# Kernel tuning notes

Measured on AMD Instinct MI355X. Metric: run time of the kernel, lower is better.

Reference implementation:

```python
import jax, jax.numpy as jnp
import numpy as np

B, LATENT, H, OUT, T, L = 4096, 128, 256, 88, 64, 5  # batch, latent, hidden, output(88 keys), seq_len, num_layers


def setup_inputs() -> dict:
    key = jax.random.key(0)
    ks = jax.random.split(key, 8)
    sc = 1.0 / np.sqrt(H)
    n = lambda k, shp, s: (jax.random.normal(k, shp, jnp.float32) * s)
    return {
        "x": jax.random.normal(ks[0], (B, LATENT), jnp.float32),
        "linear_w": n(ks[1], (H, LATENT), 1.0 / np.sqrt(LATENT)),
        "linear_b": jnp.zeros((H,), jnp.float32),
        # PyTorch LSTM layout: [4H, in] with gate order i, f, g, o. Layer-0 input size == H.
        "w_ih": n(ks[2], (L, 4 * H, H), sc),
        "w_hh": n(ks[3], (L, 4 * H, H), sc),
        "b_ih": n(ks[4], (L, 4 * H), sc),
        "b_hh": n(ks[5], (L, 4 * H), sc),
        "out_w": n(ks[6], (OUT, H), sc),
        "out_b": jnp.zeros((OUT,), jnp.float32),
    }


def _lstm_cell(gates, c):
    # gates: [B, 4H] pre-activation, PyTorch order i, f, g, o
    i, f, g, o = jnp.split(gates, 4, axis=-1)
    c_new = jax.nn.sigmoid(f) * c + jax.nn.sigmoid(i) * jnp.tanh(g)
    h_new = jax.nn.sigmoid(o) * jnp.tanh(c_new)
    return h_new, c_new


def _lstm(xp, w_ih, w_hh, b_ih, b_hh):
    # xp: [B, H] latent projection, repeated over T timesteps (constant input).
    bsz = xp.shape[0]
    gx0 = xp @ w_ih[0].T + b_ih[0]  # layer-0 input gates, constant across time [B, 4H]
    h0 = jnp.zeros((L, bsz, H), xp.dtype)
    c0 = jnp.zeros((L, bsz, H), xp.dtype)

    def step(carry, _):
        h, c = carry  # [L, B, H]
        hs, cs = [], []
        layer_in_gates = gx0
        for l in range(L):  # fixed small loop over structurally distinct layers
            if l > 0:
                layer_in_gates = hs[-1] @ w_ih[l].T + b_ih[l]
            gates = layer_in_gates + h[l] @ w_hh[l].T + b_hh[l]
            hl, cl = _lstm_cell(gates, c[l])
            hs.append(hl)
            cs.append(cl)
        return (jnp.stack(hs), jnp.stack(cs)), hs[-1]

    _, ys = jax.lax.scan(step, (h0, c0), None, length=T)  # ys: [T, B, H]
    return ys.transpose(1, 0, 2)  # [B, T, H]


def reference(x, linear_w, linear_b, w_ih, w_hh, b_ih, b_hh, out_w, out_b):
    xp = x @ linear_w.T + linear_b  # [B, H]; unsqueeze+repeat folded into constant gx0
    y = _lstm(xp, w_ih, w_hh, b_ih, b_hh)  # [B, T, H]
    return jax.nn.sigmoid(y @ out_w.T + out_b)  # [B, T, OUT]
```

## Files before the change

### kernel.cpp

```cpp
#include <hip/hip_runtime.h>
#include <hip/hip_bf16.h>
#include <cstdint>

#define B_ 4096
#define H_ 256
#define G_ 1024
#define T_ 64
#define L_ 5

typedef __hip_bfloat16 bf16;
typedef __bf16 bf16x8 __attribute__((ext_vector_type(8)));
typedef float f32x4 __attribute__((ext_vector_type(4)));

#define OFF_WCOMB   0ull
#define OFF_WIH0R   5242880ull
#define OFF_LWT     5767168ull
#define OFF_XB      5832704ull
#define OFF_OBW     6881280ull
#define OFF_BIAS    6930432ull
#define OFF_W1      6950912ull
#define OFF_B0X     7213056ull
#define OFF_H0      25825280ull
#define OFF_H1      34213888ull
#define OFF_C1      42602496ull
#define OFF_YS      63574016ull
#define OFF_C0      199888896ull
#define TOTAL_WS    220860416ull
#define ZERO_BYTES  31457280ull
#define SLOT_H      2097152ull
#define SLOT_C      4194304ull

__device__ __forceinline__ bf16* h_ptr(char* ws, int l, int p) {
  return (bf16*)(ws + (p ? OFF_H1 : OFF_H0) + (size_t)l * SLOT_H);
}
__device__ __forceinline__ float* c_ptr(char* ws, int l, int p) {
  return (float*)(ws + (p ? OFF_C1 : OFF_C0) + (size_t)l * SLOT_C);
}
__device__ __forceinline__ bf16* ys_ptr(char* ws, int s) {
  return (bf16*)(ws + OFF_YS + (size_t)s * SLOT_H);
}

__device__ __forceinline__ float frcp(float x) { return __builtin_amdgcn_rcpf(x); }
__device__ __forceinline__ float fsig(float x) { return frcp(1.0f + __expf(-x)); }
__device__ __forceinline__ float ftanh(float x) { return 1.0f - 2.0f * frcp(1.0f + __expf(2.0f * x)); }

__device__ __forceinline__ void gload16(const void* g, void* l) {
  __builtin_amdgcn_global_load_lds((const __attribute__((address_space(1))) void*)g,
                                   (__attribute__((address_space(3))) void*)l, 16, 0, 0);
}

__device__ __forceinline__ void stage_tile(char* dst, const bf16* src, long stride, int koff,
                                           int wv, int lane) {
#pragma unroll
  for (int i = 0; i < 4; ++i) {
    int r = 32 * wv + 8 * i + (lane >> 3);
    int cb = ((lane & 7) << 4) ^ ((r & 7) << 4);
    const bf16* g = src + (long)r * stride + koff + (cb >> 1);
    char* ld = dst + (32 * wv + 8 * i) * 128;
    gload16(g, ld);
  }
}

template <int OUTMODE>
__device__ void gemm_core(const bf16* __restrict__ A1, long lda1,
                          const bf16* __restrict__ B1, long ldw1, int nkb1,
                          const bf16* __restrict__ A2, long lda2,
                          const bf16* __restrict__ B2, long ldw2, int nkb2,
                          const float* __restrict__ bias,
                          bf16* __restrict__ outB, int ldo,
                          const float* __restrict__ cIn, float* __restrict__ cOut,
                          bf16* __restrict__ hOut,
                          int mtile, int ntile, char* smem) {
  const int tid = threadIdx.x;
  const int lane = tid & 63, wv = tid >> 6;
  const int wrow = wv >> 1, wcol = wv & 1;
  const int row0 = mtile * 128;
  const int n0 = ntile * 128;

  char* As[2] = { smem,          smem + 16384 };
  char* Bs[2] = { smem + 32768,  smem + 49152 };

  f32x4 acc[4][4];
#pragma unroll
  for (int n = 0; n < 4; n++) {
    int col = n0 + wcol * 64 + 16 * n + (lane & 15);
    float bv = bias ? bias[col] : 0.0f;
#pragma unroll
    for (int m = 0; m < 4; m++)
#pragma unroll
      for (int r = 0; r < 4; r++) acc[m][n][r] = bv;
  }

  const int nkb = nkb1 + nkb2;
  stage_tile(As[0], A1 + (long)row0 * lda1, lda1, 0, wv, lane);
  stage_tile(Bs[0], B1 + (long)n0 * ldw1, ldw1, 0, wv, lane);

  for (int kb = 0; kb < nkb; ++kb) {
    __syncthreads();
    if (kb + 1 < nkb) {
      int k2 = kb + 1, b = k2 & 1;
      if (k2 < nkb1) {
        stage_tile(As[b], A1 + (long)row0 * lda1, lda1, k2 * 64, wv, lane);
        stage_tile(Bs[b], B1 + (long)n0 * ldw1, ldw1, k2 * 64, wv, lane);
      } else {
        stage_tile(As[b], A2 + (long)row0 * lda2, lda2, (k2 - nkb1) * 64, wv, lane);
        stage_tile(Bs[b], B2 + (long)n0 * ldw2, ldw2, (k2 - nkb1) * 64, wv, lane);
      }
    }
    char* Ab = As[kb & 1]; char* Bb = Bs[kb & 1];
#pragma unroll
    for (int ks = 0; ks < 2; ++ks) {
      bf16x8 af[4], bfr[4];
#pragma unroll
      for (int m = 0; m < 4; m++) {
        int r = wrow * 64 + 16 * m + (lane & 15);
        int cb = (ks * 64 + ((lane >> 4) << 4)) ^ ((r & 7) << 4);
        af[m] = *(const bf16x8*)(Ab + r * 128 + cb);
      }
#pragma unroll
      for (int n = 0; n < 4; n++) {
        int r = wcol * 64 + 16 * n + (lane & 15);
        int cb = (ks * 64 + ((lane >> 4) << 4)) ^ ((r & 7) << 4);
        bfr[n] = *(const bf16x8*)(Bb + r * 128 + cb);
      }
#pragma unroll
      for (int m = 0; m < 4; m++)
#pragma unroll
        for (int n = 0; n < 4; n++)
          acc[m][n] = __builtin_amdgcn_mfma_f32_16x16x32_bf16(af[m], bfr[n], acc[m][n], 0, 0, 0);
    }
  }
  __syncthreads();

  if (OUTMODE == 1) {
#pragma unroll
    for (int m = 0; m < 4; m++)
#pragma unroll
      for (int n = 0; n < 4; n++)
#pragma unroll
        for (int r = 0; r < 4; r++) {
          int row = row0 + wrow * 64 + 16 * m + ((lane >> 4) << 2) + r;
          int col = n0 + wcol * 64 + 16 * n + (lane & 15);
          outB[(long)row * ldo + col] = __float2bfloat16(acc[m][n][r]);
        }
  } else {
#pragma unroll
    for (int m = 0; m < 4; m++)
#pragma unroll
      for (int n = 0; n < 4; n++)
#pragma unroll
        for (int r = 0; r < 4; r++) {
          int rr = wrow * 64 + 16 * m + ((lane >> 4) << 2) + r;
          int cc = wcol * 64 + 16 * n + (lane & 15);
          int byte = (rr << 9) + (((cc << 2)) ^ ((rr & 7) << 4));
          *(float*)(smem + byte) = acc[m][n][r];
        }
    __syncthreads();
    int j = tid & 31;
    int rbase = tid >> 5;
#pragma unroll
    for (int i = 0; i < 16; i++) {
      int rr = rbase + 8 * i;
      int byte = (rr << 9) + ((j << 4) ^ ((rr & 7) << 4));
      f32x4 g4 = *(const f32x4*)(smem + byte);
      int row = row0 + rr;
      int jj = ntile * 32 + j;
      float cold = cIn[(long)row * H_ + jj];
      float cn = fsig(g4[1]) * cold + fsig(g4[0]) * ftanh(g4[2]);
      float hn = fsig(g4[3]) * ftanh(cn);
      cOut[(long)row * H_ + jj] = cn;
      hOut[(long)row * H_ + jj] = __float2bfloat16(hn);
    }
  }
}

__global__ __launch_bounds__(256) void gemm_bf16out(const bf16* A1, long lda1,
                                                    const bf16* B1, long ldw1, int nkb1,
                                                    bf16* outB, int ldo) {
  __shared__ __align__(16) char smem[65536];
  int mtile = blockIdx.x & 31;
  int ntile = blockIdx.x >> 5;
  gemm_core<1>(A1, lda1, B1, ldw1, nkb1, A1, lda1, B1, ldw1, 0,
               nullptr, outB, ldo, nullptr, nullptr, nullptr, mtile, ntile, smem);
}

__global__ __launch_bounds__(256) void lstm_diag(int d, char* __restrict__ ws) {
  __shared__ __align__(16) char smem[65536];
  int l0 = d > 63 ? d - 63 : 0;
  int l = l0 + blockIdx.y;
  int t = d - l;
  int mtile = blockIdx.x & 31;
  int ntile = blockIdx.x >> 5;
  int sp = (t & 1) ^ 1, op = t & 1;

  const bf16* xb = (const bf16*)(ws + OFF_XB);
  const bf16* W1 = (const bf16*)(ws + OFF_W1);
  const bf16* wc = (const bf16*)(ws + OFF_WCOMB) + (long)l * G_ * 512;

  const bf16 *A1, *A2, *B1, *B2;
  long lda1, lda2, ldw1, ldw2;
  int nkb1, nkb2;
  const float* bias;

  if (l == 0) {
    bias = (const float*)(ws + OFF_B0X);
    if (t == 0) {
      A1 = xb; lda1 = 128; B1 = W1; ldw1 = 128; nkb1 = 2;
      A2 = xb; lda2 = 128; B2 = W1; ldw2 = 128; nkb2 = 0;
    } else {
      A1 = h_ptr(ws, 0, sp); lda1 = 256; B1 = wc; ldw1 = 512; nkb1 = 4;
      A2 = xb; lda2 = 128; B2 = W1; ldw2 = 128; nkb2 = 2;
    }
  } else {
    bias = (const float*)(ws + OFF_BIAS) + l * G_;
    A1 = h_ptr(ws, l - 1, op); lda1 = 256; B1 = wc; ldw1 = 512; nkb1 = 4;
    A2 = (l == 4) ? ys_ptr(ws, t) : h_ptr(ws, l, sp); lda2 = 256;
    B2 = wc + 256; ldw2 = 512; nkb2 = 4;
  }
  const float* cIn = c_ptr(ws, l, sp);
  float* cOut = c_ptr(ws, l, op);
  bf16* hOut = (l == 4) ? ys_ptr(ws, t + 1) : h_ptr(ws, l, op);

  gemm_core<2>(A1, lda1, B1, ldw1, nkb1, A2, lda2, B2, ldw2, nkb2,
               bias, nullptr, 0, cIn, cOut, hOut, mtile, ntile, smem);
}

__global__ __launch_bounds__(256) void proj_kernel(char* __restrict__ ws,
                                                   const float* __restrict__ ob,
                                                   float* __restrict__ out) {
  __shared__ __align__(16) char smem[49152];
  int mtile = blockIdx.x;
  int t = blockIdx.y;
  const bf16* ys = ys_ptr(ws, t + 1);
  const char* obw = (const char*)(ws + OFF_OBW);
  int tid = threadIdx.x, lane = tid & 63, wv = tid >> 6;
#pragma unroll
  for (int i = 0; i < 12; i++) {
    int r = wv * 24 + i * 2 + (lane >> 5);
    int cb = ((lane & 31) << 4) ^ ((r & 7) << 4);
    gload16(obw + r * 512 + cb, smem + (wv * 24 + i * 2) * 512);
  }
  __syncthreads();
  f32x4 acc[2][6];
#pragma unroll
  for (int m = 0; m < 2; m++)
#pragma unroll
    for (int n = 0; n < 6; n++)
#pragma unroll
      for (int r = 0; r < 4; r++) acc[m][n][r] = 0.0f;
  const char* arow = (const char*)(ys + (long)(mtile * 128) * 256);
  for (int kk = 0; kk < 256; kk += 32) {
    bf16x8 af[2], bfr[6];
#pragma unroll
    for (int m = 0; m < 2; m++) {
      int r = wv * 32 + 16 * m + (lane & 15);
      af[m] = *(const bf16x8*)(arow + (long)r * 512 + kk * 2 + ((lane >> 4) << 4));
    }
#pragma unroll
    for (int n = 0; n < 6; n++) {
      int r = 16 * n + (lane & 15);
      int cb = (kk * 2 + ((lane >> 4) << 4)) ^ ((r & 7) << 4);
      bfr[n] = *(const bf16x8*)(smem + r * 512 + cb);
    }
#pragma unroll
    for (int m = 0; m < 2; m++)
#pragma unroll
      for (int n = 0; n < 6; n++)
        acc[m][n] = __builtin_amdgcn_mfma_f32_16x16x32_bf16(af[m], bfr[n], acc[m][n], 0, 0, 0);
  }
#pragma unroll
  for (int m = 0; m < 2; m++)
#pragma unroll
    for (int n = 0; n < 6; n++)
#pragma unroll
      for (int r = 0; r < 4; r++) {
        int row = mtile * 128 + wv * 32 + 16 * m + ((lane >> 4) << 2) + r;
        int o = 16 * n + (lane & 15);
        if (o < 88) {
          float v = acc[m][n][r] + ob[o];
          out[((long)row * T_ + t) * 88 + o] = fsig(v);
        }
      }
}

__global__ void prep_kernel(const float* __restrict__ x, const float* __restrict__ lw,
                            const float* __restrict__ wih, const float* __restrict__ whh,
                            const float* __restrict__ bih, const float* __restrict__ bhh,
                            const float* __restrict__ ow, char* __restrict__ ws) {
  bf16* xb = (bf16*)(ws + OFF_XB);
  bf16* lwt = (bf16*)(ws + OFF_LWT);
  bf16* wcomb = (bf16*)(ws + OFF_WCOMB);
  bf16* wih0r = (bf16*)(ws + OFF_WIH0R);
  bf16* obw = (bf16*)(ws + OFF_OBW);
  float* bias = (float*)(ws + OFF_BIAS);
  const int S0 = 524288, S1 = 32768, S2 = 2621440, S3 = 262144, S4 = 24576, S5 = 5120;
  const int total = S0 + S1 + S2 + S3 + S4 + S5;
  for (int i = blockIdx.x * blockDim.x + threadIdx.x; i < total; i += gridDim.x * blockDim.x) {
    int idx = i;
    if (idx < S0) { xb[idx] = __float2bfloat16(x[idx]); continue; }
    idx -= S0;
    if (idx < S1) {
      int r = idx >> 8, c = idx & 255;
      lwt[idx] = __float2bfloat16(lw[c * 128 + r]); continue;
    }
    idx -= S1;
    if (idx < S2) {
      int l = idx >> 19;
      int rem = idx & 524287;
      int n = rem >> 9;
      int k = rem & 511;
      int row = (n & 3) * 256 + (n >> 2);
      float v;
      if (l == 0) v = (k < 256) ? whh[row * 256 + k] : 0.0f;
      else        v = (k < 256) ? wih[(l * 1024 + row) * 256 + k]
                                : whh[(l * 1024 + row) * 256 + (k - 256)];
      wcomb[idx] = __float2bfloat16(v); continue;
    }
    idx -= S2;
    if (idx < S3) {
      int n = idx >> 8, k = idx & 255;
      int row = (n & 3) * 256 + (n >> 2);
      wih0r[idx] = __float2bfloat16(wih[row * 256 + k]); continue;
    }
    idx -= S3;
    if (idx < S4) {
      int r = idx >> 8, k = idx & 255;
      obw[idx] = __float2bfloat16(r < 88 ? ow[r * 256 + k] : 0.0f); continue;
    }
    idx -= S4;
    {
      int l = idx >> 10, n = idx & 1023;
      int row = (n & 3) * 256 + (n >> 2);
      bias[idx] = bih[l * 1024 + row] + bhh[l * 1024 + row];
    }
  }
}

__global__ void bias_fix_kernel(const float* __restrict__ lb, char* __restrict__ ws) {
  int n = blockIdx.x * blockDim.x + threadIdx.x;
  if (n >= 1024) return;
  const bf16* wih0r = (const bf16*)(ws + OFF_WIH0R) + (long)n * 256;
  const float* biasS = (const float*)(ws + OFF_BIAS);
  float s = biasS[n];
  for (int k = 0; k < 256; ++k) s += __bfloat162float(wih0r[k]) * lb[k];
  ((float*)(ws + OFF_B0X))[n] = s;
}

extern "C" void kernel_launch(void* const* d_in, const int* in_sizes, int n_in,
                              void* d_out, int out_size, void* d_ws, size_t ws_size,
                              hipStream_t stream) {
  const float* x   = (const float*)d_in[0];
  const float* lw  = (const float*)d_in[1];
  const float* lb  = (const float*)d_in[2];
  const float* wih = (const float*)d_in[3];
  const float* whh = (const float*)d_in[4];
  const float* bih = (const float*)d_in[5];
  const float* bhh = (const float*)d_in[6];
  const float* ow  = (const float*)d_in[7];
  const float* ob  = (const float*)d_in[8];
  char* ws = (char*)d_ws;
  float* out = (float*)d_out;

  if (ws_size < TOTAL_WS) return;

  hipMemsetAsync(ws + OFF_H1, 0, ZERO_BYTES, stream);
  prep_kernel<<<2048, 256, 0, stream>>>(x, lw, wih, whh, bih, bhh, ow, ws);

  gemm_bf16out<<<dim3(8), 256, 0, stream>>>(
      (const bf16*)(ws + OFF_WIH0R), 256, (const bf16*)(ws + OFF_LWT), 256, 4,
      (bf16*)(ws + OFF_W1), 128);

  bias_fix_kernel<<<4, 256, 0, stream>>>(lb, ws);

  for (int d = 0; d < 68; ++d) {
    int lo = d > 63 ? d - 63 : 0;
    int hi = d < 4 ? d : 4;
    int nc = hi - lo + 1;
    lstm_diag<<<dim3(256, nc), 256, 0, stream>>>(d, ws);
  }

  proj_kernel<<<dim3(32, 64), 256, 0, stream>>>(ws, ob, out);
}
```

Measured before the change: 2.634 ms.

## Enlarge LSTM GEMM tiles to 256x256 and fuse cell epilogue via lane shuffles

The fused gate GEMM plus LSTM cell moves from 128x128 tiles with 256 threads to 256x256 tiles with 512 threads and 128KB of LDS. This raises operand reuse per block and cuts the diagonal-wavefront grid from 256 to 64 blocks per layer. The LDS round-trip in the cell epilogue is replaced by register shuffles that gather the four interleaved gates into each lane. The W1 projection is padded to 256 columns and the workspace offsets are recompacted to match. The fewer, larger blocks may leave many CUs idle on a 256-CU GPU, and the higher register pressure may lower occupancy.

```diff
diff --git a/kernel.cpp b/kernel.cpp
--- a/kernel.cpp
+++ b/kernel.cpp
@@ -15,17 +15,17 @@
 #define OFF_WCOMB   0ull
 #define OFF_WIH0R   5242880ull
 #define OFF_LWT     5767168ull
-#define OFF_XB      5832704ull
-#define OFF_OBW     6881280ull
-#define OFF_BIAS    6930432ull
-#define OFF_W1      6950912ull
-#define OFF_B0X     7213056ull
-#define OFF_H0      25825280ull
-#define OFF_H1      34213888ull
-#define OFF_C1      42602496ull
-#define OFF_YS      63574016ull
-#define OFF_C0      199888896ull
-#define TOTAL_WS    220860416ull
+#define OFF_XB      5898240ull
+#define OFF_OBW     6946816ull
+#define OFF_BIAS    6995968ull
+#define OFF_W1      7016448ull
+#define OFF_B0X     7540736ull
+#define OFF_H0      8388608ull
+#define OFF_H1      16777216ull
+#define OFF_C1      25165824ull
+#define OFF_YS      46137344ull
+#define OFF_C0      182452224ull
+#define TOTAL_WS    203423744ull
 #define ZERO_BYTES  31457280ull
 #define SLOT_H      2097152ull
 #define SLOT_C      4194304ull
@@ -53,10 +53,10 @@
                                            int wv, int lane) {
 #pragma unroll
   for (int i = 0; i < 4; ++i) {
-    int r = 32 * wv + 8 * i + (lane >> 3);
+    int r = i * 64 + wv * 8 + (lane >> 3);
     int cb = ((lane & 7) << 4) ^ ((r & 7) << 4);
     const bf16* g = src + (long)r * stride + koff + (cb >> 1);
-    char* ld = dst + (32 * wv + 8 * i) * 128;
+    char* ld = dst + (i * 64 + wv * 8) * 128;
     gload16(g, ld);
   }
 }
@@ -74,16 +74,16 @@
   const int tid = threadIdx.x;
   const int lane = tid & 63, wv = tid >> 6;
   const int wrow = wv >> 1, wcol = wv & 1;
-  const int row0 = mtile * 128;
-  const int n0 = ntile * 128;
-
-  char* As[2] = { smem,          smem + 16384 };
-  char* Bs[2] = { smem + 32768,  smem + 49152 };
-
-  f32x4 acc[4][4];
-#pragma unroll
-  for (int n = 0; n < 4; n++) {
-    int col = n0 + wcol * 64 + 16 * n + (lane & 15);
+  const int row0 = mtile * 256;
+  const int n0 = ntile * 256;
+
+  char* As[2] = { smem,          smem + 32768 };
+  char* Bs[2] = { smem + 65536,  smem + 98304 };
+
+  f32x4 acc[4][8];
+#pragma unroll
+  for (int n = 0; n < 8; n++) {
+    int col = n0 + wcol * 128 + 16 * n + (lane & 15);
     float bv = bias ? bias[col] : 0.0f;
 #pragma unroll
     for (int m = 0; m < 4; m++)
@@ -110,7 +110,7 @@
     char* Ab = As[kb & 1]; char* Bb = Bs[kb & 1];
 #pragma unroll
     for (int ks = 0; ks < 2; ++ks) {
-      bf16x8 af[4], bfr[4];
+      bf16x8 af[4];
 #pragma unroll
       for (int m = 0; m < 4; m++) {
         int r = wrow * 64 + 16 * m + (lane & 15);
@@ -118,79 +118,69 @@
         af[m] = *(const bf16x8*)(Ab + r * 128 + cb);
       }
 #pragma unroll
-      for (int n = 0; n < 4; n++) {
-        int r = wcol * 64 + 16 * n + (lane & 15);
+      for (int n = 0; n < 8; n++) {
+        int r = wcol * 128 + 16 * n + (lane & 15);
         int cb = (ks * 64 + ((lane >> 4) << 4)) ^ ((r & 7) << 4);
-        bfr[n] = *(const bf16x8*)(Bb + r * 128 + cb);
-      }
-#pragma unroll
-      for (int m = 0; m < 4; m++)
-#pragma unroll
-        for (int n = 0; n < 4; n++)
-          acc[m][n] = __builtin_amdgcn_mfma_f32_16x16x32_bf16(af[m], bfr[n], acc[m][n], 0, 0, 0);
-    }
-  }
-  __syncthreads();
+        bf16x8 bfr = *(const bf16x8*)(Bb + r * 128 + cb);
+#pragma unroll
+        for (int m = 0; m < 4; m++)
+          acc[m][n] = __builtin_amdgcn_mfma_f32_16x16x32_bf16(af[m], bfr, acc[m][n], 0, 0, 0);
+      }
+    }
+  }
 
   if (OUTMODE == 1) {
 #pragma unroll
     for (int m = 0; m < 4; m++)
 #pragma unroll
-      for (int n = 0; n < 4; n++)
+      for (int n = 0; n < 8; n++)
 #pragma unroll
         for (int r = 0; r < 4; r++) {
           int row = row0 + wrow * 64 + 16 * m + ((lane >> 4) << 2) + r;
-          int col = n0 + wcol * 64 + 16 * n + (lane & 15);
+          int col = n0 + wcol * 128 + 16 * n + (lane & 15);
           outB[(long)row * ldo + col] = __float2bfloat16(acc[m][n][r]);
         }
   } else {
 #pragma unroll
     for (int m = 0; m < 4; m++)
 #pragma unroll
-      for (int n = 0; n < 4; n++)
-#pragma unroll
-        for (int r = 0; r < 4; r++) {
-          int rr = wrow * 64 + 16 * m + ((lane >> 4) << 2) + r;
-          int cc = wcol * 64 + 16 * n + (lane & 15);
-          int byte = (rr << 9) + (((cc << 2)) ^ ((rr & 7) << 4));
-          *(float*)(smem + byte) = acc[m][n][r];
-        }
-    __syncthreads();
-    int j = tid & 31;
-    int rbase = tid >> 5;
-#pragma unroll
-    for (int i = 0; i < 16; i++) {
-      int rr = rbase + 8 * i;
-      int byte = (rr << 9) + ((j << 4) ^ ((rr & 7) << 4));
-      f32x4 g4 = *(const f32x4*)(smem + byte);
-      int row = row0 + rr;
-      int jj = ntile * 32 + j;
-      float cold = cIn[(long)row * H_ + jj];
-      float cn = fsig(g4[1]) * cold + fsig(g4[0]) * ftanh(g4[2]);
-      float hn = fsig(g4[3]) * ftanh(cn);
-      cOut[(long)row * H_ + jj] = cn;
-      hOut[(long)row * H_ + jj] = __float2bfloat16(hn);
-    }
-  }
-}
-
-__global__ __launch_bounds__(256) void gemm_bf16out(const bf16* A1, long lda1,
-                                                    const bf16* B1, long ldw1, int nkb1,
-                                                    bf16* outB, int ldo) {
-  __shared__ __align__(16) char smem[65536];
-  int mtile = blockIdx.x & 31;
-  int ntile = blockIdx.x >> 5;
+      for (int n = 0; n < 8; n++) {
+        f32x4 v = acc[m][n];
+        f32x4 t;
+        t[0] = __shfl_xor(v[0], 2); t[1] = __shfl_xor(v[1], 2);
+        t[2] = __shfl_xor(v[2], 2); t[3] = __shfl_xor(v[3], 2);
+        if ((lane & 2) == 0) { v[2] = t[0]; v[3] = t[1]; }
+        else                 { v[0] = t[2]; v[1] = t[3]; }
+        t[0] = __shfl_xor(v[0], 1); t[1] = __shfl_xor(v[1], 1);
+        t[2] = __shfl_xor(v[2], 1); t[3] = __shfl_xor(v[3], 1);
+        if ((lane & 1) == 0) { v[1] = t[0]; v[3] = t[2]; }
+        else                 { v[0] = t[1]; v[2] = t[3]; }
+        int row = row0 + wrow * 64 + 16 * m + ((lane >> 4) << 2) + (lane & 3);
+        int j   = ntile * 64 + wcol * 32 + 4 * n + ((lane >> 2) & 3);
+        float cold = cIn[(long)row * H_ + j];
+        float cn = fsig(v[1]) * cold + fsig(v[0]) * ftanh(v[2]);
+        float hn = fsig(v[3]) * ftanh(cn);
+        cOut[(long)row * H_ + j] = cn;
+        hOut[(long)row * H_ + j] = __float2bfloat16(hn);
+      }
+  }
+}
+
+__global__ __launch_bounds__(512, 2) void gemm_bf16out(const bf16* A1, long lda1,
+                                                       const bf16* B1, long ldw1, int nkb1,
+                                                       bf16* outB, int ldo) {
+  __shared__ __align__(16) char smem[131072];
   gemm_core<1>(A1, lda1, B1, ldw1, nkb1, A1, lda1, B1, ldw1, 0,
-               nullptr, outB, ldo, nullptr, nullptr, nullptr, mtile, ntile, smem);
-}
-
-__global__ __launch_bounds__(256) void lstm_diag(int d, char* __restrict__ ws) {
-  __shared__ __align__(16) char smem[65536];
+               nullptr, outB, ldo, nullptr, nullptr, nullptr, blockIdx.x, 0, smem);
+}
+
+__global__ __launch_bounds__(512, 2) void lstm_diag(int d, char* __restrict__ ws) {
+  __shared__ __align__(16) char smem[131072];
   int l0 = d > 63 ? d - 63 : 0;
   int l = l0 + blockIdx.y;
   int t = d - l;
-  int mtile = blockIdx.x & 31;
-  int ntile = blockIdx.x >> 5;
+  int mtile = blockIdx.x & 15;
+  int ntile = blockIdx.x >> 4;
   int sp = (t & 1) ^ 1, op = t & 1;
 
   const bf16* xb = (const bf16*)(ws + OFF_XB);
@@ -205,11 +195,11 @@
   if (l == 0) {
     bias = (const float*)(ws + OFF_B0X);
     if (t == 0) {
-      A1 = xb; lda1 = 128; B1 = W1; ldw1 = 128; nkb1 = 2;
-      A2 = xb; lda2 = 128; B2 = W1; ldw2 = 128; nkb2 = 0;
+      A1 = xb; lda1 = 128; B1 = W1; ldw1 = 256; nkb1 = 2;
+      A2 = xb; lda2 = 128; B2 = W1; ldw2 = 256; nkb2 = 0;
     } else {
       A1 = h_ptr(ws, 0, sp); lda1 = 256; B1 = wc; ldw1 = 512; nkb1 = 4;
-      A2 = xb; lda2 = 128; B2 = W1; ldw2 = 128; nkb2 = 2;
+      A2 = xb; lda2 = 128; B2 = W1; ldw2 = 256; nkb2 = 2;
     }
   } else {
     bias = (const float*)(ws + OFF_BIAS) + l * G_;
@@ -293,7 +283,7 @@
   bf16* wih0r = (bf16*)(ws + OFF_WIH0R);
   bf16* obw = (bf16*)(ws + OFF_OBW);
   float* bias = (float*)(ws + OFF_BIAS);
-  const int S0 = 524288, S1 = 32768, S2 = 2621440, S3 = 262144, S4 = 24576, S5 = 5120;
+  const int S0 = 524288, S1 = 65536, S2 = 2621440, S3 = 262144, S4 = 24576, S5 = 5120;
   const int total = S0 + S1 + S2 + S3 + S4 + S5;
   for (int i = blockIdx.x * blockDim.x + threadIdx.x; i < total; i += gridDim.x * blockDim.x) {
     int idx = i;
@@ -301,7 +291,7 @@
     idx -= S0;
     if (idx < S1) {
       int r = idx >> 8, c = idx & 255;
-      lwt[idx] = __float2bfloat16(lw[c * 128 + r]); continue;
+      lwt[idx] = __float2bfloat16(r < 128 ? lw[c * 128 + r] : 0.0f); continue;
     }
     idx -= S1;
     if (idx < S2) {
@@ -366,9 +356,9 @@
   hipMemsetAsync(ws + OFF_H1, 0, ZERO_BYTES, stream);
   prep_kernel<<<2048, 256, 0, stream>>>(x, lw, wih, whh, bih, bhh, ow, ws);
 
-  gemm_bf16out<<<dim3(8), 256, 0, stream>>>(
+  gemm_bf16out<<<dim3(4), 512, 0, stream>>>(
       (const bf16*)(ws + OFF_WIH0R), 256, (const bf16*)(ws + OFF_LWT), 256, 4,
-      (bf16*)(ws + OFF_W1), 128);
+      (bf16*)(ws + OFF_W1), 256);
 
   bias_fix_kernel<<<4, 256, 0, stream>>>(lb, ws);
 
@@ -376,7 +366,7 @@
     int lo = d > 63 ? d - 63 : 0;
     int hi = d < 4 ? d : 4;
     int nc = hi - lo + 1;
-    lstm_diag<<<dim3(256, nc), 256, 0, stream>>>(d, ws);
+    lstm_diag<<<dim3(64, nc), 512, 0, stream>>>(d, ws);
   }
 
   proj_kernel<<<dim3(32, 64), 256, 0, stream>>>(ws, ob, out);
```

Measured after the change: 3.389 ms. 1.29x slower.
